# Kernel tuning notes

Measured on AMD Instinct MI355X. Metric: run time of the kernel, lower is better.

Reference implementation:

```python
import jax, jax.numpy as jnp
import numpy as np

H = 512; W = 512; C_IN = 14; HID = 128; N_CELLS = 8192

def _rn(k, shape, sc=0.05):
    return jax.random.normal(k, shape, jnp.float32) * sc

def setup_inputs() -> dict:
    key = jax.random.key(0)
    ks = jax.random.split(key, 32)
    inp = {
        'x': jax.random.normal(ks[0], (1, C_IN, H, W), jnp.float32),
        'cell_i': jax.random.randint(ks[1], (N_CELLS,), 0, H, jnp.int32),
        'cell_j': jax.random.randint(ks[2], (N_CELLS,), 0, W, jnp.int32),
        'action': jax.random.randint(ks[3], (N_CELLS, 4), 0, 2, jnp.int32),
        'w1': _rn(ks[4], (48, C_IN, 3, 3)), 'b1': _rn(ks[5], (48,)),
        'g1': jnp.ones((48,), jnp.float32), 'be1': jnp.zeros((48,), jnp.float32),
        'w2': _rn(ks[6], (96, 48, 3, 3)), 'b2': _rn(ks[7], (96,)),
        'g2': jnp.ones((96,), jnp.float32), 'be2': jnp.zeros((96,), jnp.float32),
        'w3': _rn(ks[8], (HID, 96, 3, 3)), 'b3': _rn(ks[9], (HID,)),
        'g3': jnp.ones((HID,), jnp.float32), 'be3': jnp.zeros((HID,), jnp.float32),
        'fw1': _rn(ks[10], (HID * 9, 256)), 'fb1': _rn(ks[11], (256,)),
        'fw2': _rn(ks[12], (256, 128)), 'fb2': _rn(ks[13], (128,)),
        'bw': _rn(ks[14], (128, 4)), 'bb': _rn(ks[15], (4,)),
        'iw': _rn(ks[16], (128, 4)), 'ib': _rn(ks[17], (4,)),
        'tw': _rn(ks[18], (128, 4)), 'tb': _rn(ks[19], (4,)),
        'vw1': _rn(ks[20], (HID, 64)), 'vb1': _rn(ks[21], (64,)),
        'vw2': _rn(ks[22], (64, 1)), 'vb2': _rn(ks[23], (1,)),
    }
    return inp

def _conv(x, w, b):
    y = jax.lax.conv_general_dilated(x, w, (1, 1), 'SAME',
                                     dimension_numbers=('NCHW', 'OIHW', 'NCHW'))
    return y + b[None, :, None, None]

def _gn(x, gamma, beta, groups, eps=1e-5):
    n, c, h, w = x.shape
    xr = x.reshape(n, groups, -1)
    m = xr.mean(axis=2, keepdims=True)
    v = xr.var(axis=2, keepdims=True)
    xn = ((xr - m) * jax.lax.rsqrt(v + eps)).reshape(n, c, h, w)
    return xn * gamma[None, :, None, None] + beta[None, :, None, None]

def _forward(x, cell_i, cell_j, action, w1, b1, g1, be1, w2, b2, g2, be2,
             w3, b3, g3, be3, fw1, fb1, fw2, fb2, bw, bb, iw, ib, tw, tb,
             vw1, vb1, vw2, vb2):
    # Encoder: conv -> GN -> ReLU x3
    f = jax.nn.relu(_gn(_conv(x, w1, b1), g1, be1, 6))
    f = jax.nn.relu(_gn(_conv(f, w2, b2), g2, be2, 12))
    f = jax.nn.relu(_gn(_conv(f, w3, b3), g3, be3, 16))  # (1, HID, H, W)
    # Value head: global avg pool -> MLP
    pooled = f.mean(axis=(2, 3))  # (1, HID)
    value = jax.nn.relu(pooled @ vw1 + vb1) @ vw2 + vb2  # (1, 1)
    # Per-burning-cell 3x3 patch gather (zero-padded borders)
    fpad = jnp.pad(f, ((0, 0), (0, 0), (1, 1), (1, 1)))[0]  # (HID, H+2, W+2)
    def slice_patch(i, j):
        return jax.lax.dynamic_slice(fpad, (0, i, j), (HID, 3, 3))
    patches = jax.vmap(slice_patch)(cell_i, cell_j)  # (N, HID, 3, 3)
    flat = patches.reshape(patches.shape[0], HID * 9)
    shared = jax.nn.relu(jax.nn.relu(flat @ fw1 + fb1) @ fw2 + fb2)  # (N, 128)
    burn_logits = shared @ bw + bb
    intensity = shared @ iw + ib
    temp = shared @ tw + tb
    p = jnp.clip(jax.nn.sigmoid(burn_logits), 1e-7, 1.0 - 1e-7)
    a = action.astype(jnp.float32)
    log_prob = jnp.sum(a * jnp.log(p) + (1.0 - a) * jnp.log(1.0 - p))
    entropy = -jnp.sum(p * jnp.log(p) + (1.0 - p) * jnp.log(1.0 - p))
    # Scatter sampled actions into grid at N/E/S/W neighbors (in-bounds only)
    di = jnp.array([-1, 0, 1, 0], jnp.int32)
    dj = jnp.array([0, 1, 0, -1], jnp.int32)
    ni = cell_i[:, None] + di
    nj = cell_j[:, None] + dj
    valid = (ni >= 0) & (ni < H) & (nj >= 0) & (nj < W) & (a > 0.5)
    grid = jnp.zeros((H, W), jnp.float32).at[
        jnp.clip(ni, 0, H - 1), jnp.clip(nj, 0, W - 1)].max(valid.astype(jnp.float32))
    return grid, log_prob, entropy, value, intensity, temp

def reference(x, cell_i, cell_j, action, w1, b1, g1, be1, w2, b2, g2, be2,
              w3, b3, g3, be3, fw1, fb1, fw2, fb2, bw, bb, iw, ib, tw, tb,
              vw1, vb1, vw2, vb2):
    return _forward(x, cell_i, cell_j, action, w1, b1, g1, be1, w2, b2, g2, be2,
                    w3, b3, g3, be3, fw1, fb1, fw2, fb2, bw, bb, iw, ib, tw, tb,
                    vw1, vb1, vw2, vb2)
```

## Files before the change

### kernel.cpp

```cpp
#include <hip/hip_runtime.h>
#include <hip/hip_bf16.h>
#include <cstddef>

#define NPIX 262144
#define PW 514
typedef __hip_bfloat16 bf16;
typedef __attribute__((ext_vector_type(8))) short short8;
typedef __attribute__((ext_vector_type(4))) float f32x4;

__device__ inline unsigned short f2bfu(float f){
  __hip_bfloat16 h = __float2bfloat16(f);
  return *(reinterpret_cast<unsigned short*>(&h));
}
__device__ inline float bflo(unsigned u){ return __uint_as_float(u<<16); }
__device__ inline float bfhi(unsigned u){ return __uint_as_float(u & 0xffff0000u); }
__device__ inline unsigned pack2bf(float a, float b){
  unsigned ua = __float_as_uint(a), ub = __float_as_uint(b);
  return ((ua + 0x8000u) >> 16) | ((ub + 0x8000u) & 0xffff0000u);
}
__device__ inline void dma16(const bf16* g, unsigned short* l){
  __builtin_amdgcn_global_load_lds(
      (const __attribute__((address_space(1))) unsigned int*)g,
      (__attribute__((address_space(3))) unsigned int*)l, 16, 0, 0);
}

__device__ inline void computeAB(const float* stats, const float* gamma, const float* beta,
                                 int c, float& A, float& B){
  int g = c >> 3;
  const float invN = 1.f/2097152.f;
  float m = stats[g*2]*invN;
  float v = stats[g*2+1]*invN - m*m;
  float inv = rsqrtf(v + 1e-5f);
  A = inv*gamma[c];
  B = beta[c] - m*A;
}

__global__ void setup_kernel(float* out, float* stats, float* pooled,
                             const float* __restrict__ w1, bf16* __restrict__ wT1,
                             const float* __restrict__ w2, bf16* __restrict__ wT2,
                             const float* __restrict__ w3, bf16* __restrict__ wT3,
                             const float* __restrict__ fw1, bf16* __restrict__ wF1T,
                             const float* __restrict__ fw2, bf16* __restrict__ wF2T){
  int b = blockIdx.x;
  if (b < 1025){
    int i = b*256 + threadIdx.x;
    if (i < 262147) out[i] = 0.f;
    if (i < 68)  stats[i]  = 0.f;
    if (i < 128) pooled[i] = 0.f;
    return;
  }
  b -= 1025;
  if (b < 30){
    int idx = b*256 + threadIdx.x;
    if (idx < 5*48*32){
      int kp = idx & 31; int oc = (idx >> 5) % 48; int kc = idx / (48*32);
      int k = kc*32 + kp;
      int tap = k >> 4, c = k & 15;
      float v = (tap < 9 && c < 14) ? w1[(oc*14 + c)*9 + tap] : 0.f;
      wT1[idx] = __float2bfloat16(v);
    }
    return;
  }
  b -= 30;
  if (b < 216){
    int idx = b*256 + threadIdx.x;
    if (idx < 9*2*96*32){
      int cp = idx & 31; int rest = idx >> 5;
      int oc = rest % 96; rest /= 96;
      int cc = rest % 2; int tap = rest / 2;
      int ic = cc*32 + cp;
      float v = (ic < 48) ? w2[(oc*48 + ic)*9 + tap] : 0.f;
      wT2[idx] = __float2bfloat16(v);
    }
    return;
  }
  b -= 216;
  if (b < 432){
    int idx = b*256 + threadIdx.x;
    if (idx < 9*3*128*32){
      int cp = idx & 31; int rest = idx >> 5;
      int oc = rest & 127; rest >>= 7;
      int cc = rest % 3; int tap = rest / 3;
      int ic = cc*32 + cp;
      float v = (ic < 96) ? w3[(oc*96 + ic)*9 + tap] : 0.f;
      wT3[idx] = __float2bfloat16(v);
    }
    return;
  }
  b -= 432;
  if (b < 1152){
    int idx = b*256 + threadIdx.x;
    if (idx < 36*256*32){
      int kp = idx & 31; int oc = (idx >> 5) & 255; int kc = idx >> 13;
      int k2 = kc*32 + kp;
      int rr = k2 >> 7, ch = k2 & 127;
      wF1T[idx] = __float2bfloat16(fw1[(size_t)(ch*9 + rr)*256 + oc]);
    }
    return;
  }
  b -= 1152;
  {
    int idx = b*256 + threadIdx.x;
    if (idx < 8*128*32){
      int kp = idx & 31; int oc = (idx >> 5) & 127; int kc = idx >> 12;
      wF2T[idx] = __float2bfloat16(fw2[(size_t)(kc*32 + kp)*128 + oc]);
    }
  }
}

__launch_bounds__(256,2)
__global__ void conv1_mfma_kernel(const float* __restrict__ x, const bf16* __restrict__ wT,
                                  const float* __restrict__ bias, bf16* __restrict__ out,
                                  float* __restrict__ stats){
  constexpr int XP = 24;
  __shared__ unsigned short sX[324*XP];
  __shared__ float sStat[96];
  const int tid = threadIdx.x;
  const int lane = tid & 63, wave = tid >> 6;
  const int quad = lane >> 4, l15 = lane & 15;
  const int tileX = (blockIdx.x & 31)*16, tileY = (blockIdx.x >> 5)*16;
  if (tid < 96) sStat[tid] = 0.f;
  for (int p = tid; p < 324; p += 256){ sX[p*XP+14] = 0; sX[p*XP+15] = 0; }
  for (int idx = tid; idx < 14*324; idx += 256){
    int c = idx / 324, p = idx - c*324;
    int r = p / 18, col = p - r*18;
    int gy = tileY + r - 1, gx = tileX + col - 1;
    float v = 0.f;
    if ((unsigned)gy < 512u && (unsigned)gx < 512u) v = x[(size_t)c*NPIX + gy*512 + gx];
    sX[p*XP + c] = f2bfu(v);
  }
  __syncthreads();

  f32x4 acc[3][4];
  #pragma unroll
  for (int t = 0; t < 3; ++t){
    f32x4 bv = *(const f32x4*)(bias + t*16 + quad*4);
    #pragma unroll
    for (int s = 0; s < 4; ++s) acc[t][s] = bv;
  }
  const int pxb = wave*4;
  const int h = quad >> 1, chalf = (quad & 1)*8;
  const int T0[5] = {0,2,4,6,8};
  const int T1[5] = {1,3,5,7,8};
  #pragma unroll
  for (int kc = 0; kc < 5; ++kc){
    short8 a[3];
    #pragma unroll
    for (int t = 0; t < 3; ++t)
      a[t] = *(const short8*)((const unsigned short*)wT + (size_t)(kc*48 + t*16 + l15)*32 + quad*8);
    const int ky = h ? (T1[kc]/3) : (T0[kc]/3);
    const int kx = h ? (T1[kc]%3) : (T0[kc]%3);
    #pragma unroll
    for (int s = 0; s < 4; ++s){
      int py = pxb + s;
      short8 bfr = *(const short8*)(&sX[((py+ky)*18 + l15+kx)*XP + chalf]);
      #pragma unroll
      for (int t = 0; t < 3; ++t)
        acc[t][s] = __builtin_amdgcn_mfma_f32_16x16x32_bf16(a[t], bfr, acc[t][s], 0, 0, 0);
    }
  }
  #pragma unroll
  for (int t = 0; t < 3; ++t){
    #pragma unroll
    for (int r = 0; r < 4; ++r){
      float sv = 0.f, sq = 0.f;
      #pragma unroll
      for (int s = 0; s < 4; ++s){ float v = acc[t][s][r]; sv += v; sq += v*v; }
      #pragma unroll
      for (int m = 1; m < 16; m <<= 1){ sv += __shfl_xor(sv, m); sq += __shfl_xor(sq, m); }
      if (l15 == 0){
        atomicAdd(&sStat[(t*16 + quad*4 + r)*2],   sv);
        atomicAdd(&sStat[(t*16 + quad*4 + r)*2+1], sq);
      }
    }
    #pragma unroll
    for (int s = 0; s < 4; ++s){
      f32x4 v = acc[t][s];
      uint2 pk;
      pk.x = pack2bf(v[0], v[1]);
      pk.y = pack2bf(v[2], v[3]);
      *(uint2*)(out + ((size_t)(tileY+pxb+s+1)*PW + tileX+l15+1)*48 + t*16 + quad*4) = pk;
    }
  }
  __syncthreads();
  if (tid < 12){
    int g = tid >> 1, wsel = tid & 1;
    float v = 0.f;
    #pragma unroll
    for (int j = 0; j < 8; ++j) v += sStat[(g*8+j)*2 + wsel];
    atomicAdd(&stats[g*2 + wsel], v);
  }
}

template<int C>
__global__ void norm_kernel(bf16* buf, const float* __restrict__ stats,
                            const float* __restrict__ gamma, const float* __restrict__ beta){
  __shared__ float sAB[2*C];
  const int tid = threadIdx.x;
  if (tid < C){ float A,B; computeAB(stats, gamma, beta, tid, A, B); sAB[tid]=A; sAB[C+tid]=B; }
  __syncthreads();
  const int y = blockIdx.x >> 2, q = blockIdx.x & 3;
  uint4* row = (uint4*)(buf + (size_t)y*PW*C);
  constexpr int NU4 = PW*C/8/4;
  const bool brow = (y == 0) | (y == 513);
  for (int i = q*NU4 + tid; i < (q+1)*NU4; i += 256){
    int e = i*8;
    int px = e / C;
    if (brow | (px == 0) | (px == 513)){ row[i] = make_uint4(0,0,0,0); continue; }
    int ch = e - px*C;
    uint4 v = row[i];
    unsigned uu[4] = {v.x,v.y,v.z,v.w}, ou[4];
    #pragma unroll
    for (int j = 0; j < 4; ++j){
      float a = fmaxf(bflo(uu[j])*sAB[ch+j*2]   + sAB[C+ch+j*2],   0.f);
      float d = fmaxf(bfhi(uu[j])*sAB[ch+j*2+1] + sAB[C+ch+j*2+1], 0.f);
      ou[j] = pack2bf(a, d);
    }
    row[i] = make_uint4(ou[0],ou[1],ou[2],ou[3]);
  }
}

template<int IC, int NCC, int OCT, int OC, int NW, int TH>
__launch_bounds__(NW*64, 3)
__global__ void conv_dma_kernel(const bf16* __restrict__ in, const bf16* __restrict__ wT,
                                const float* __restrict__ bias,
                                bf16* __restrict__ out, float* __restrict__ outstats){
  constexpr int NT   = NW*64;
  constexpr int ROWS = TH + 2;
  constexpr int SLOTS = ROWS * 72;
  constexpr int K    = (SLOTS + NT - 1) / NT;
  constexpr int REM  = SLOTS - (K-1)*NT;
  __shared__ unsigned short sIn[2][SLOTS*8];
  __shared__ float sStat[2*OC];
  const int tid  = threadIdx.x;
  const int lane = tid & 63, wave = tid >> 6;
  const int quad = lane >> 4, l15 = lane & 15;
  const int tileX = (blockIdx.x & 31) * 16, tileY = (blockIdx.x >> 5) * TH;
  const int ocbase = wave * (OCT*16);

  for (int i = tid; i < 2*OC; i += NT) sStat[i] = 0.f;

  unsigned off[K];
  #pragma unroll
  for (int k = 0; k < K; ++k){
    int slot = tid + k*NT;
    if (k < K-1 || tid < REM){
      int row = slot/72; int rem = slot - row*72;
      int cc = rem/18;   int col = rem - cc*18;
      off[k] = (unsigned)(((tileY+row)*PW + tileX+col)*IC + cc*8);
    }
  }
  auto issueDMA = [&](int cr, int bi){
    #pragma unroll
    for (int k = 0; k < K; ++k){
      if (k == K-1 && tid >= REM) continue;
      dma16(in + off[k] + cr*32, &sIn[bi][(tid + k*NT)*8]);
    }
  };

  f32x4 acc[OCT][TH];
  #pragma unroll
  for (int t = 0; t < OCT; ++t){
    f32x4 bv = *(const f32x4*)(bias + ocbase + t*16 + quad*4);
    #pragma unroll
    for (int s = 0; s < TH; ++s) acc[t][s] = bv;
  }

  issueDMA(0, 0);
  __syncthreads();

  #pragma unroll 1
  for (int cr = 0; cr < NCC; ++cr){
    if (cr + 1 < NCC) issueDMA(cr + 1, (cr + 1) & 1);
    const unsigned short* B0 = &sIn[cr & 1][(quad*18 + l15)*8];
    const unsigned short* W0 = (const unsigned short*)wT + ((size_t)cr*OC + ocbase + l15)*32 + quad*8;

    #pragma unroll
    for (int kx = 0; kx < 3; ++kx){
      short8 a[3][OCT];
      #pragma unroll
      for (int ky = 0; ky < 3; ++ky)
        #pragma unroll
        for (int t = 0; t < OCT; ++t)
          a[ky][t] = *(const short8*)(W0 + (size_t)(ky*3+kx)*(NCC*OC*32) + t*512);
      #pragma unroll
      for (int r = 0; r < ROWS; ++r){
        short8 b = *(const short8*)(B0 + (r*72 + kx)*8);
        #pragma unroll
        for (int ky = 0; ky < 3; ++ky){
          const int s = r - ky;
          if (s >= 0 && s < TH){
            #pragma unroll
            for (int t = 0; t < OCT; ++t)
              acc[t][s] = __builtin_amdgcn_mfma_f32_16x16x32_bf16(a[ky][t], b, acc[t][s], 0, 0, 0);
          }
        }
      }
    }
    __syncthreads();
  }

  #pragma unroll
  for (int t = 0; t < OCT; ++t){
    #pragma unroll
    for (int r = 0; r < 4; ++r){
      float sv = 0.f, sq = 0.f;
      #pragma unroll
      for (int s = 0; s < TH; ++s){ float v = acc[t][s][r]; sv += v; sq += v*v; }
      #pragma unroll
      for (int m = 1; m < 16; m <<= 1){ sv += __shfl_xor(sv, m); sq += __shfl_xor(sq, m); }
      if (l15 == 0){
        atomicAdd(&sStat[(ocbase + t*16 + quad*4 + r)*2],   sv);
        atomicAdd(&sStat[(ocbase + t*16 + quad*4 + r)*2+1], sq);
      }
    }
    #pragma unroll
    for (int s = 0; s < TH; ++s){
      f32x4 v = acc[t][s];
      uint2 pk;
      pk.x = pack2bf(v[0], v[1]);
      pk.y = pack2bf(v[2], v[3]);
      *(uint2*)(out + ((size_t)(tileY+s+1)*PW + (tileX+l15+1))*OC + ocbase + t*16 + quad*4) = pk;
    }
  }
  __syncthreads();
  if (tid < (OC/8)*2){
    int g = tid >> 1, wsel = tid & 1;
    float v = 0.f;
    #pragma unroll
    for (int j = 0; j < 8; ++j) v += sStat[(g*8+j)*2 + wsel];
    atomicAdd(&outstats[g*2 + wsel], v);
  }
}

__launch_bounds__(256)
__global__ void mega_kernel(const bf16* __restrict__ f, const float* __restrict__ instats,
                            const float* __restrict__ gamma, const float* __restrict__ beta,
                            const int* __restrict__ cell_i, const int* __restrict__ cell_j,
                            const int* __restrict__ action,
                            const bf16* __restrict__ wT, const float* __restrict__ fb1,
                            const bf16* __restrict__ wT2, const float* __restrict__ fb2,
                            const float* __restrict__ bw, const float* __restrict__ bb,
                            const float* __restrict__ iw, const float* __restrict__ ib,
                            const float* __restrict__ tw, const float* __restrict__ tb,
                            float* __restrict__ pooled, float* __restrict__ out){
  constexpr int KST = 1160;
  __shared__ unsigned short sG[16*KST];
  __shared__ unsigned short h1L[16*264];
  __shared__ float sAB[256];
  __shared__ int sij[32];
  __shared__ float sRed[2];
  __shared__ float sP[128];
  float* h2L = (float*)sG;
  const int tid = threadIdx.x;
  const int lane = tid & 63, wave = tid >> 6;
  const int quad = lane >> 4, l15 = lane & 15;
  const int cb = blockIdx.x*16;

  if (tid < 2) sRed[tid] = 0.f;
  if (tid < 128){ float A,B; computeAB(instats, gamma, beta, tid, A, B);
    sAB[tid]=A; sAB[128+tid]=B; sP[tid]=0.f; }
  if (tid < 16) sij[tid] = cell_i[cb + tid];
  else if (tid < 32) sij[tid] = cell_j[cb + tid - 16];
  __syncthreads();

  for (int idx = tid; idx < 16*144; idx += 256){
    int c8 = idx & 15; int t2 = idx >> 4;
    int cell = t2 / 9, rr = t2 - cell*9;
    int r = rr/3, cl = rr - r*3;
    int py = sij[cell] + r, px = sij[16+cell] + cl;
    uint4 v = *(const uint4*)(f + ((size_t)py*PW + px)*128 + c8*8);
    bool border = (py==0) | (py==513) | (px==0) | (px==513);
    unsigned uu[4] = {v.x, v.y, v.z, v.w};
    unsigned ou[4];
    #pragma unroll
    for (int j = 0; j < 4; ++j){
      int ch = c8*8 + j*2;
      float a = border ? 0.f : fmaxf(bflo(uu[j])*sAB[ch]   + sAB[128+ch],   0.f);
      float d = border ? 0.f : fmaxf(bfhi(uu[j])*sAB[ch+1] + sAB[128+ch+1], 0.f);
      ou[j] = pack2bf(a, d);
    }
    uint4 wv; wv.x = ou[0]; wv.y = ou[1]; wv.z = ou[2]; wv.w = ou[3];
    *(uint4*)(&sG[cell*KST + rr*128 + c8*8]) = wv;
  }
  __syncthreads();

  {
    f32x4 acc[4];
    const int ocb = wave*64;
    #pragma unroll
    for (int t = 0; t < 4; ++t)
      acc[t] = *(const f32x4*)(fb1 + ocb + t*16 + quad*4);
    #pragma unroll 2
    for (int kc = 0; kc < 36; ++kc){
      short8 b = *(const short8*)(&sG[l15*KST + kc*32 + quad*8]);
      #pragma unroll
      for (int t = 0; t < 4; ++t){
        short8 a = *(const short8*)((const unsigned short*)wT + ((size_t)kc*256 + ocb + t*16 + l15)*32 + quad*8);
        acc[t] = __builtin_amdgcn_mfma_f32_16x16x32_bf16(a, b, acc[t], 0, 0, 0);
      }
    }
    #pragma unroll
    for (int t = 0; t < 4; ++t){
      f32x4 v = acc[t];
      uint2 pk;
      pk.x = pack2bf(fmaxf(v[0],0.f), fmaxf(v[1],0.f));
      pk.y = pack2bf(fmaxf(v[2],0.f), fmaxf(v[3],0.f));
      *(uint2*)(&h1L[l15*264 + ocb + t*16 + quad*4]) = pk;
    }
  }
  __syncthreads();

  {
    const int och = wave*32;
    f32x4 acc2[2];
    #pragma unroll
    for (int t = 0; t < 2; ++t)
      acc2[t] = *(const f32x4*)(fb2 + och + t*16 + quad*4);
    #pragma unroll
    for (int kc = 0; kc < 8; ++kc){
      short8 b = *(const short8*)(&h1L[l15*264 + kc*32 + quad*8]);
      #pragma unroll
      for (int t = 0; t < 2; ++t){
        short8 a = *(const short8*)((const unsigned short*)wT2 + ((size_t)kc*128 + och + t*16 + l15)*32 + quad*8);
        acc2[t] = __builtin_amdgcn_mfma_f32_16x16x32_bf16(a, b, acc2[t], 0, 0, 0);
      }
    }
    #pragma unroll
    for (int t = 0; t < 2; ++t){
      f32x4 v = acc2[t];
      #pragma unroll
      for (int r = 0; r < 4; ++r) v[r] = fmaxf(v[r], 0.f);
      *(f32x4*)(&h2L[l15*132 + och + t*16 + quad*4]) = v;
    }
  }
  __syncthreads();

  if (tid < 192){
    int cell = tid/12, jj = tid - cell*12;
    int which = jj >> 2, o = jj & 3;
    const float* W  = (which==0) ? bw : (which==1 ? iw : tw);
    const float* Bp = (which==0) ? bb : (which==1 ? ib : tb);
    float d = Bp[o];
    const float* h2 = &h2L[cell*132];
    for (int k = 0; k < 128; k++) d += h2[k]*W[k*4+o];
    int cellg = cb + cell;
    if (which == 1){
      out[262147 + cellg*4 + o] = d;
    } else if (which == 2){
      out[262147 + 32768 + cellg*4 + o] = d;
    } else {
      float p = 1.f/(1.f + __expf(-d));
      p = fminf(fmaxf(p, 1e-7f), 1.f - 1e-7f);
      int a = action[cellg*4 + o];
      float lp  = a ? __logf(p) : __logf(1.f-p);
      float ent = -(p*__logf(p) + (1.f-p)*__logf(1.f-p));
      atomicAdd(&sRed[0], lp);
      atomicAdd(&sRed[1], ent);
      if (a){
        const int di[4] = {-1,0,1,0};
        const int dj[4] = {0,1,0,-1};
        int ni = sij[cell] + di[o];
        int nj = sij[16+cell] + dj[o];
        if ((unsigned)ni < 512u && (unsigned)nj < 512u)
          out[ni*512 + nj] = 1.0f;
      }
    }
  }

  {
    const int gl = tid & 15, xl = tid >> 4;
    float A[8], B[8];
    #pragma unroll
    for (int j = 0; j < 8; ++j){ A[j] = sAB[gl*8+j]; B[j] = sAB[128+gl*8+j]; }
    const int y = blockIdx.x;
    float ps[8] = {0,0,0,0,0,0,0,0};
    for (int x2 = xl; x2 < 512; x2 += 16){
      uint4 v = *(const uint4*)(f + ((size_t)(y+1)*PW + x2+1)*128 + gl*8);
      unsigned uu[4] = {v.x, v.y, v.z, v.w};
      #pragma unroll
      for (int j = 0; j < 4; ++j){
        ps[j*2]   += fmaxf(bflo(uu[j])*A[j*2]   + B[j*2],   0.f);
        ps[j*2+1] += fmaxf(bfhi(uu[j])*A[j*2+1] + B[j*2+1], 0.f);
      }
    }
    #pragma unroll
    for (int j = 0; j < 8; ++j) atomicAdd(&sP[gl*8+j], ps[j]);
  }
  __syncthreads();
  if (tid == 0){
    atomicAdd(&out[262144], sRed[0]);
    atomicAdd(&out[262145], sRed[1]);
  }
  if (tid < 128) atomicAdd(&pooled[tid], sP[tid]);
}

__global__ void value_kernel(const float* __restrict__ pooled, const float* __restrict__ vw1,
                             const float* __restrict__ vb1, const float* __restrict__ vw2,
                             const float* __restrict__ vb2, float* __restrict__ out){
  int t = threadIdx.x;
  float h = vb1[t];
  const float invN = 1.f/262144.f;
  for (int c = 0; c < 128; c++) h += (pooled[c]*invN)*vw1[c*64+t];
  h = fmaxf(h, 0.f);
  float v = h*vw2[t];
  #pragma unroll
  for (int off = 32; off; off >>= 1) v += __shfl_xor(v, off);
  if (t == 0) out[262146] = v + vb2[0];
}

extern "C" void kernel_launch(void* const* d_in, const int* in_sizes, int n_in,
                              void* d_out, int out_size, void* d_ws, size_t ws_size,
                              hipStream_t stream) {
  (void)in_sizes; (void)n_in; (void)out_size; (void)ws_size;
  const float* x      = (const float*)d_in[0];
  const int*  cell_i  = (const int*)d_in[1];
  const int*  cell_j  = (const int*)d_in[2];
  const int*  action  = (const int*)d_in[3];
  const float* w1 = (const float*)d_in[4];  const float* b1 = (const float*)d_in[5];
  const float* g1 = (const float*)d_in[6];  const float* be1= (const float*)d_in[7];
  const float* w2 = (const float*)d_in[8];  const float* b2 = (const float*)d_in[9];
  const float* g2 = (const float*)d_in[10]; const float* be2= (const float*)d_in[11];
  const float* w3 = (const float*)d_in[12]; const float* b3 = (const float*)d_in[13];
  const float* g3 = (const float*)d_in[14]; const float* be3= (const float*)d_in[15];
  const float* fw1= (const float*)d_in[16]; const float* fb1= (const float*)d_in[17];
  const float* fw2= (const float*)d_in[18]; const float* fb2= (const float*)d_in[19];
  const float* bw = (const float*)d_in[20]; const float* bb = (const float*)d_in[21];
  const float* iw = (const float*)d_in[22]; const float* ib = (const float*)d_in[23];
  const float* tw = (const float*)d_in[24]; const float* tb = (const float*)d_in[25];
  const float* vw1= (const float*)d_in[26]; const float* vb1= (const float*)d_in[27];
  const float* vw2= (const float*)d_in[28]; const float* vb2= (const float*)d_in[29];

  float* out = (float*)d_out;
  char* ws = (char*)d_ws;
  bf16* buf1 = (bf16*)(ws);
  bf16* buf2 = (bf16*)(ws + 25362816);
  bf16* bufF = (bf16*)(ws + 76088448);
  bf16* wT2  = (bf16*)(ws + 143722624);
  bf16* wT3  = (bf16*)(ws + 143833216);
  bf16* wT1  = (bf16*)(ws + 144054400);
  bf16* wF1T = (bf16*)(ws + 144069760);
  bf16* wF2T = (bf16*)(ws + 144659584);
  float* statsf = (float*)(ws + 144725120);
  float* pooled = statsf + 128;

  setup_kernel<<<2983, 256, 0, stream>>>(out, statsf, pooled, w1, wT1, w2, wT2, w3, wT3,
                                         fw1, wF1T, fw2, wF2T);
  conv1_mfma_kernel<<<1024, 256, 0, stream>>>(x, wT1, b1, buf1, statsf + 0);
  norm_kernel<48><<<514*4, 256, 0, stream>>>(buf1, statsf + 0, g1, be1);
  conv_dma_kernel<48,2,2,96,3,8><<<2048, 192, 0, stream>>>(buf1, wT2, b2, buf2, statsf + 12);
  norm_kernel<96><<<514*4, 256, 0, stream>>>(buf2, statsf + 12, g2, be2);
  conv_dma_kernel<96,3,2,128,4,8><<<2048, 256, 0, stream>>>(buf2, wT3, b3, bufF, statsf + 36);
  mega_kernel<<<512, 256, 0, stream>>>(bufF, statsf + 36, g3, be3, cell_i, cell_j, action,
                                       wF1T, fb1, wF2T, fb2, bw, bb, iw, ib, tw, tb,
                                       pooled, out);
  value_kernel<<<1, 64, 0, stream>>>(pooled, vw1, vb1, vw2, vb2, out);
}
```

Before: 361.2 us.

## Fuse GroupNorm+ReLU into conv input loading, drop separate norm kernels

Removes the two standalone norm_kernel passes and applies the GroupNorm affine and ReLU to the input tile while it is staged into LDS inside the conv kernels. The async global_load_lds DMA is replaced by register loads, a transform, and LDS stores, with the chunk loop manually pipelined and s_setprio raised around the MFMA section. Border zeroing moves into setup_kernel, and padding pixels are forced to zero during staging. This saves two full read-modify-write passes over the large activation buffers, at the cost of higher register pressure, extra ALU work per conv tile, and losing the asynchronous DMA path. Occupancy for conv2 is lowered to 2.

Measured after the change: 439.6 us. 1.22x slower.

```diff
diff --git a/kernel.cpp b/kernel.cpp
--- a/kernel.cpp
+++ b/kernel.cpp
@@ -17,11 +17,6 @@
 __device__ inline unsigned pack2bf(float a, float b){
   unsigned ua = __float_as_uint(a), ub = __float_as_uint(b);
   return ((ua + 0x8000u) >> 16) | ((ub + 0x8000u) & 0xffff0000u);
-}
-__device__ inline void dma16(const bf16* g, unsigned short* l){
-  __builtin_amdgcn_global_load_lds(
-      (const __attribute__((address_space(1))) unsigned int*)g,
-      (__attribute__((address_space(3))) unsigned int*)l, 16, 0, 0);
 }
 
 __device__ inline void computeAB(const float* stats, const float* gamma, const float* beta,
@@ -40,7 +35,8 @@
                              const float* __restrict__ w2, bf16* __restrict__ wT2,
                              const float* __restrict__ w3, bf16* __restrict__ wT3,
                              const float* __restrict__ fw1, bf16* __restrict__ wF1T,
-                             const float* __restrict__ fw2, bf16* __restrict__ wF2T){
+                             const float* __restrict__ fw2, bf16* __restrict__ wF2T,
+                             bf16* __restrict__ bufB1, bf16* __restrict__ bufB2){
   int b = blockIdx.x;
   if (b < 1025){
     int i = b*256 + threadIdx.x;
@@ -99,11 +95,41 @@
     return;
   }
   b -= 1152;
-  {
+  if (b < 128){
     int idx = b*256 + threadIdx.x;
     if (idx < 8*128*32){
       int kp = idx & 31; int oc = (idx >> 5) & 127; int kc = idx >> 12;
       wF2T[idx] = __float2bfloat16(fw2[(size_t)(kc*32 + kp)*128 + oc]);
+    }
+    return;
+  }
+  b -= 128;
+  {
+    int u = b*256 + threadIdx.x;
+    const uint4 z = make_uint4(0u,0u,0u,0u);
+    if (u < 6168){
+      int row = (u < 3084) ? 0 : 513; int r2 = (u < 3084) ? u : u - 3084;
+      ((uint4*)bufB1)[(size_t)row*3084 + r2] = z;
+      return;
+    }
+    u -= 6168;
+    if (u < 6144){
+      int p = u/6, q = u - p*6;
+      int y = 1 + (p>>1), xx = (p&1) ? 513 : 0;
+      ((uint4*)(bufB1 + ((size_t)y*PW + xx)*48))[q] = z;
+      return;
+    }
+    u -= 6144;
+    if (u < 12336){
+      int row = (u < 6168) ? 0 : 513; int r2 = (u < 6168) ? u : u - 6168;
+      ((uint4*)bufB2)[(size_t)row*6168 + r2] = z;
+      return;
+    }
+    u -= 12336;
+    if (u < 12288){
+      int p = u/12, q = u - p*12;
+      int y = 1 + (p>>1), xx = (p&1) ? 513 : 0;
+      ((uint4*)(bufB2 + ((size_t)y*PW + xx)*96))[q] = z;
     }
   }
 }
@@ -192,46 +218,23 @@
   }
 }
 
-template<int C>
-__global__ void norm_kernel(bf16* buf, const float* __restrict__ stats,
-                            const float* __restrict__ gamma, const float* __restrict__ beta){
-  __shared__ float sAB[2*C];
-  const int tid = threadIdx.x;
-  if (tid < C){ float A,B; computeAB(stats, gamma, beta, tid, A, B); sAB[tid]=A; sAB[C+tid]=B; }
-  __syncthreads();
-  const int y = blockIdx.x >> 2, q = blockIdx.x & 3;
-  uint4* row = (uint4*)(buf + (size_t)y*PW*C);
-  constexpr int NU4 = PW*C/8/4;
-  const bool brow = (y == 0) | (y == 513);
-  for (int i = q*NU4 + tid; i < (q+1)*NU4; i += 256){
-    int e = i*8;
-    int px = e / C;
-    if (brow | (px == 0) | (px == 513)){ row[i] = make_uint4(0,0,0,0); continue; }
-    int ch = e - px*C;
-    uint4 v = row[i];
-    unsigned uu[4] = {v.x,v.y,v.z,v.w}, ou[4];
-    #pragma unroll
-    for (int j = 0; j < 4; ++j){
-      float a = fmaxf(bflo(uu[j])*sAB[ch+j*2]   + sAB[C+ch+j*2],   0.f);
-      float d = fmaxf(bfhi(uu[j])*sAB[ch+j*2+1] + sAB[C+ch+j*2+1], 0.f);
-      ou[j] = pack2bf(a, d);
-    }
-    row[i] = make_uint4(ou[0],ou[1],ou[2],ou[3]);
-  }
-}
-
-template<int IC, int NCC, int OCT, int OC, int NW, int TH>
-__launch_bounds__(NW*64, 3)
+template<int IC, int NCC, int OCT, int OC, int NW, int TH, int MINW>
+__launch_bounds__(NW*64, MINW)
 __global__ void conv_dma_kernel(const bf16* __restrict__ in, const bf16* __restrict__ wT,
                                 const float* __restrict__ bias,
+                                const float* __restrict__ instats,
+                                const float* __restrict__ gamma, const float* __restrict__ beta,
                                 bf16* __restrict__ out, float* __restrict__ outstats){
   constexpr int NT   = NW*64;
   constexpr int ROWS = TH + 2;
   constexpr int SLOTS = ROWS * 72;
   constexpr int K    = (SLOTS + NT - 1) / NT;
   constexpr int REM  = SLOTS - (K-1)*NT;
+  constexpr int CPAD = NCC*32;
+  static_assert(NCC >= 2 && NCC <= 3, "NCC in {2,3}");
   __shared__ unsigned short sIn[2][SLOTS*8];
   __shared__ float sStat[2*OC];
+  __shared__ __align__(16) float sAB2[2*CPAD];
   const int tid  = threadIdx.x;
   const int lane = tid & 63, wave = tid >> 6;
   const int quad = lane >> 4, l15 = lane & 15;
@@ -239,22 +242,52 @@
   const int ocbase = wave * (OCT*16);
 
   for (int i = tid; i < 2*OC; i += NT) sStat[i] = 0.f;
-
-  unsigned off[K];
+  for (int c = tid; c < CPAD; c += NT){
+    float A = 0.f, B = 0.f;
+    if (c < IC) computeAB(instats, gamma, beta, c, A, B);
+    sAB2[2*c] = A; sAB2[2*c+1] = B;
+  }
+
+  unsigned off[K]; int cb2[K]; bool bflag[K];
   #pragma unroll
   for (int k = 0; k < K; ++k){
     int slot = tid + k*NT;
     if (k < K-1 || tid < REM){
       int row = slot/72; int rem = slot - row*72;
       int cc = rem/18;   int col = rem - cc*18;
-      off[k] = (unsigned)(((tileY+row)*PW + tileX+col)*IC + cc*8);
-    }
-  }
-  auto issueDMA = [&](int cr, int bi){
+      int py = tileY + row, px = tileX + col;
+      off[k]   = (unsigned)((py*PW + px)*IC + cc*8);
+      cb2[k]   = cc*16;
+      bflag[k] = (py==0) | (py==513) | (px==0) | (px==513);
+    }
+  }
+
+  uint4 rgA[K], rgB[K];
+  auto issueLoad = [&](int cr, uint4* rg){
     #pragma unroll
     for (int k = 0; k < K; ++k){
       if (k == K-1 && tid >= REM) continue;
-      dma16(in + off[k] + cr*32, &sIn[bi][(tid + k*NT)*8]);
+      rg[k] = *(const uint4*)(in + off[k] + cr*32);
+    }
+  };
+  auto doTransform = [&](int cr, const uint4* rg, int bi){
+    #pragma unroll
+    for (int k = 0; k < K; ++k){
+      if (k == K-1 && tid >= REM) continue;
+      uint4 v = rg[k];
+      unsigned uu[4] = {v.x, v.y, v.z, v.w};
+      unsigned ou[4];
+      const float* ab = &sAB2[cb2[k] + cr*64];
+      #pragma unroll
+      for (int j = 0; j < 4; ++j){
+        f32x4 abv = *(const f32x4*)(ab + j*4);
+        float a = fmaxf(bflo(uu[j])*abv[0] + abv[1], 0.f);
+        float d = fmaxf(bfhi(uu[j])*abv[2] + abv[3], 0.f);
+        ou[j] = pack2bf(a, d);
+      }
+      uint4 wv = bflag[k] ? make_uint4(0u,0u,0u,0u)
+                          : make_uint4(ou[0],ou[1],ou[2],ou[3]);
+      *(uint4*)(&sIn[bi][(tid + k*NT)*8]) = wv;
     }
   };
 
@@ -266,15 +299,10 @@
     for (int s = 0; s < TH; ++s) acc[t][s] = bv;
   }
 
-  issueDMA(0, 0);
-  __syncthreads();
-
-  #pragma unroll 1
-  for (int cr = 0; cr < NCC; ++cr){
-    if (cr + 1 < NCC) issueDMA(cr + 1, (cr + 1) & 1);
-    const unsigned short* B0 = &sIn[cr & 1][(quad*18 + l15)*8];
+  auto computeChunk = [&](int cr, int bi){
+    const unsigned short* B0 = &sIn[bi][(quad*18 + l15)*8];
     const unsigned short* W0 = (const unsigned short*)wT + ((size_t)cr*OC + ocbase + l15)*32 + quad*8;
-
+    __builtin_amdgcn_s_setprio(1);
     #pragma unroll
     for (int kx = 0; kx < 3; ++kx){
       short8 a[3][OCT];
@@ -297,8 +325,24 @@
         }
       }
     }
-    __syncthreads();
-  }
+    __builtin_amdgcn_s_setprio(0);
+  };
+
+  issueLoad(0, rgA);
+  if (NCC > 1) issueLoad(1, rgB);
+  __syncthreads();
+  doTransform(0, rgA, 0);
+  if (NCC > 2) issueLoad(2, rgA);
+  __syncthreads();
+  if (NCC > 1) doTransform(1, rgB, 1);
+  computeChunk(0, 0);
+  if (NCC > 1) __syncthreads();
+  if (NCC > 1){
+    if (NCC > 2) doTransform(2, rgA, 0);
+    computeChunk(1, 1);
+    if (NCC > 2) __syncthreads();
+  }
+  if (NCC > 2) computeChunk(2, 0);
 
   #pragma unroll
   for (int t = 0; t < OCT; ++t){
@@ -544,13 +588,13 @@
   float* statsf = (float*)(ws + 144725120);
   float* pooled = statsf + 128;
 
-  setup_kernel<<<2983, 256, 0, stream>>>(out, statsf, pooled, w1, wT1, w2, wT2, w3, wT3,
-                                         fw1, wF1T, fw2, wF2T);
+  setup_kernel<<<3128, 256, 0, stream>>>(out, statsf, pooled, w1, wT1, w2, wT2, w3, wT3,
+                                         fw1, wF1T, fw2, wF2T, buf1, buf2);
   conv1_mfma_kernel<<<1024, 256, 0, stream>>>(x, wT1, b1, buf1, statsf + 0);
-  norm_kernel<48><<<514*4, 256, 0, stream>>>(buf1, statsf + 0, g1, be1);
-  conv_dma_kernel<48,2,2,96,3,8><<<2048, 192, 0, stream>>>(buf1, wT2, b2, buf2, statsf + 12);
-  norm_kernel<96><<<514*4, 256, 0, stream>>>(buf2, statsf + 12, g2, be2);
-  conv_dma_kernel<96,3,2,128,4,8><<<2048, 256, 0, stream>>>(buf2, wT3, b3, bufF, statsf + 36);
+  conv_dma_kernel<48,2,2,96,3,8,2><<<2048, 192, 0, stream>>>(buf1, wT2, b2, statsf + 0, g1, be1,
+                                                             buf2, statsf + 12);
+  conv_dma_kernel<96,3,2,128,4,8,3><<<2048, 256, 0, stream>>>(buf2, wT3, b3, statsf + 12, g2, be2,
+                                                              bufF, statsf + 36);
   mega_kernel<<<512, 256, 0, stream>>>(bufF, statsf + 36, g3, be3, cell_i, cell_j, action,
                                        wF1T, fb1, wF2T, fb2, bw, bb, iw, ib, tw, tb,
                                        pooled, out);
```

## Prefetch all channel chunks upfront with vmcnt waits instead of double buffering

Applied to the files above, without the earlier changes.

The conv kernel now allocates one LDS buffer per channel chunk (NCC of them) and issues every global-to-LDS DMA at the start. It then waits on partial vmcnt counts and uses barriers that skip the drain before computing each chunk, so later loads overlap with earlier compute and the per-iteration full syncthreads is gone. In exchange it uses more LDS, which may lower occupancy, and the hand-set vmcnt values must match the number of outstanding loads per thread (K per chunk). That matching only holds if no other global loads are in flight, yet the weight loads in computeChunk are also global loads and count toward vmcnt.

After: 352.3 us. 2.5% less time.

```diff
diff --git a/kernel.cpp b/kernel.cpp
--- a/kernel.cpp
+++ b/kernel.cpp
@@ -22,6 +22,17 @@
   __builtin_amdgcn_global_load_lds(
       (const __attribute__((address_space(1))) unsigned int*)g,
       (__attribute__((address_space(3))) unsigned int*)l, 16, 0, 0);
+}
+template<int N> __device__ inline void waitvm(){
+  if constexpr (N == 0) asm volatile("s_waitcnt vmcnt(0)" ::: "memory");
+  else if constexpr (N == 3) asm volatile("s_waitcnt vmcnt(3)" ::: "memory");
+  else if constexpr (N == 4) asm volatile("s_waitcnt vmcnt(4)" ::: "memory");
+  else if constexpr (N == 6) asm volatile("s_waitcnt vmcnt(6)" ::: "memory");
+  else static_assert(N == 0, "unsupported vmcnt");
+}
+__device__ inline void barrier_nodrain(){
+  __builtin_amdgcn_s_barrier();
+  asm volatile("" ::: "memory");
 }
 
 __device__ inline void computeAB(const float* stats, const float* gamma, const float* beta,
@@ -230,7 +241,8 @@
   constexpr int SLOTS = ROWS * 72;
   constexpr int K    = (SLOTS + NT - 1) / NT;
   constexpr int REM  = SLOTS - (K-1)*NT;
-  __shared__ unsigned short sIn[2][SLOTS*8];
+  static_assert(NCC >= 2 && NCC <= 3, "NCC in {2,3}");
+  __shared__ unsigned short sIn[NCC][SLOTS*8];
   __shared__ float sStat[2*OC];
   const int tid  = threadIdx.x;
   const int lane = tid & 63, wave = tid >> 6;
@@ -250,11 +262,11 @@
       off[k] = (unsigned)(((tileY+row)*PW + tileX+col)*IC + cc*8);
     }
   }
-  auto issueDMA = [&](int cr, int bi){
+  auto issueDMA = [&](int cr){
     #pragma unroll
     for (int k = 0; k < K; ++k){
       if (k == K-1 && tid >= REM) continue;
-      dma16(in + off[k] + cr*32, &sIn[bi][(tid + k*NT)*8]);
+      dma16(in + off[k] + cr*32, &sIn[cr][(tid + k*NT)*8]);
     }
   };
 
@@ -266,15 +278,9 @@
     for (int s = 0; s < TH; ++s) acc[t][s] = bv;
   }
 
-  issueDMA(0, 0);
-  __syncthreads();
-
-  #pragma unroll 1
-  for (int cr = 0; cr < NCC; ++cr){
-    if (cr + 1 < NCC) issueDMA(cr + 1, (cr + 1) & 1);
-    const unsigned short* B0 = &sIn[cr & 1][(quad*18 + l15)*8];
+  auto computeChunk = [&](int cr){
+    const unsigned short* B0 = &sIn[cr][(quad*18 + l15)*8];
     const unsigned short* W0 = (const unsigned short*)wT + ((size_t)cr*OC + ocbase + l15)*32 + quad*8;
-
     #pragma unroll
     for (int kx = 0; kx < 3; ++kx){
       short8 a[3][OCT];
@@ -297,7 +303,24 @@
         }
       }
     }
-    __syncthreads();
+  };
+
+  issueDMA(0);
+  issueDMA(1);
+  if constexpr (NCC > 2) issueDMA(2);
+
+  waitvm<K*(NCC-1)>();
+  barrier_nodrain();
+  computeChunk(0);
+
+  waitvm<K*(NCC-2)>();
+  barrier_nodrain();
+  computeChunk(1);
+
+  if constexpr (NCC > 2){
+    waitvm<0>();
+    barrier_nodrain();
+    computeChunk(2);
   }
 
   #pragma unroll
```

## Use 16-row tiles with a 2x2 wave split for the second conv

Applied to the files above, without the earlier changes.

Adds a conv kernel variant for conv2 that processes 16x16 pixel tiles per block. Four waves are split into two output-channel groups of 48 channels and two 8-row pixel halves, with double-buffered DMA staging of the input halo. The larger tile lowers the halo overhead (18 rows loaded for 16 rather than 10 for 8) and halves the number of blocks. In exchange it uses more registers and LDS per block (launch bound of 2 blocks per CU), which may reduce occupancy. The old kernel is renamed and still used for conv3.

New measurement: 353.2 us, median of 3. 2.2% less time.

```diff
diff --git a/kernel.cpp b/kernel.cpp
--- a/kernel.cpp
+++ b/kernel.cpp
@@ -220,11 +220,114 @@
   }
 }
 
+template<int IC, int NCC, int OCT, int OC>
+__launch_bounds__(256, 2)
+__global__ void conv_dma16_kernel(const bf16* __restrict__ in, const bf16* __restrict__ wT,
+                                  const float* __restrict__ bias,
+                                  bf16* __restrict__ out, float* __restrict__ outstats){
+  __shared__ unsigned short sIn[2][1296*8];
+  __shared__ float sStat[2*OC];
+  const int tid  = threadIdx.x;
+  const int lane = tid & 63, wave = tid >> 6;
+  const int quad = lane >> 4, l15 = lane & 15;
+  const int ocg = wave >> 1, pxg = wave & 1;
+  const int tileX = (blockIdx.x & 31) * 16, tileY = (blockIdx.x >> 5) * 16;
+  const int ocbase = ocg * (OCT*16);
+
+  for (int i = tid; i < 2*OC; i += 256) sStat[i] = 0.f;
+
+  unsigned off[6];
+  #pragma unroll
+  for (int k = 0; k < 6; ++k){
+    int slot = tid + k*256;
+    if (k < 5 || tid < 16){
+      int row = slot/72; int rem = slot - row*72;
+      int cc = rem/18;   int col = rem - cc*18;
+      off[k] = (unsigned)(((tileY+row)*PW + tileX+col)*IC + cc*8);
+    }
+  }
+  auto issueDMA = [&](int cr, int bi){
+    #pragma unroll
+    for (int k = 0; k < 6; ++k){
+      if (k == 5 && tid >= 16) continue;
+      dma16(in + off[k] + cr*32, &sIn[bi][(tid + k*256)*8]);
+    }
+  };
+
+  f32x4 acc[OCT][8];
+  #pragma unroll
+  for (int t = 0; t < OCT; ++t){
+    f32x4 bv = *(const f32x4*)(bias + ocbase + t*16 + quad*4);
+    #pragma unroll
+    for (int s = 0; s < 8; ++s) acc[t][s] = bv;
+  }
+
+  issueDMA(0, 0);
+  __syncthreads();
+
+  #pragma unroll 1
+  for (int cr = 0; cr < NCC; ++cr){
+    const unsigned short* B0 = &sIn[cr & 1][(((pxg*8)*4 + quad)*18 + l15)*8];
+    const unsigned short* W0 = (const unsigned short*)wT + ((size_t)cr*OC + ocbase + l15)*32 + quad*8;
+
+    #pragma unroll
+    for (int tap = 0; tap < 9; ++tap){
+      if (tap == 7 && cr + 1 < NCC) issueDMA(cr + 1, (cr + 1) & 1);
+      const int ky = tap/3, kx = tap - ky*3;
+      short8 a[OCT];
+      #pragma unroll
+      for (int t = 0; t < OCT; ++t)
+        a[t] = *(const short8*)(W0 + (size_t)tap*(NCC*OC*32) + t*512);
+      #pragma unroll
+      for (int s = 0; s < 8; ++s){
+        short8 b = *(const short8*)(B0 + ((s+ky)*72 + kx)*8);
+        #pragma unroll
+        for (int t = 0; t < OCT; ++t)
+          acc[t][s] = __builtin_amdgcn_mfma_f32_16x16x32_bf16(a[t], b, acc[t][s], 0, 0, 0);
+      }
+    }
+    __syncthreads();
+  }
+
+  #pragma unroll
+  for (int t = 0; t < OCT; ++t){
+    #pragma unroll
+    for (int r = 0; r < 4; ++r){
+      float sv = 0.f, sq = 0.f;
+      #pragma unroll
+      for (int s = 0; s < 8; ++s){ float v = acc[t][s][r]; sv += v; sq += v*v; }
+      #pragma unroll
+      for (int m = 1; m < 16; m <<= 1){ sv += __shfl_xor(sv, m); sq += __shfl_xor(sq, m); }
+      if (l15 == 0){
+        atomicAdd(&sStat[(ocbase + t*16 + quad*4 + r)*2],   sv);
+        atomicAdd(&sStat[(ocbase + t*16 + quad*4 + r)*2+1], sq);
+      }
+    }
+    #pragma unroll
+    for (int s = 0; s < 8; ++s){
+      int py = pxg*8 + s;
+      f32x4 v = acc[t][s];
+      uint2 pk;
+      pk.x = pack2bf(v[0], v[1]);
+      pk.y = pack2bf(v[2], v[3]);
+      *(uint2*)(out + ((size_t)(tileY+py+1)*PW + (tileX+l15+1))*OC + ocbase + t*16 + quad*4) = pk;
+    }
+  }
+  __syncthreads();
+  if (tid < (OC/8)*2){
+    int g = tid >> 1, wsel = tid & 1;
+    float v = 0.f;
+    #pragma unroll
+    for (int j = 0; j < 8; ++j) v += sStat[(g*8+j)*2 + wsel];
+    atomicAdd(&outstats[g*2 + wsel], v);
+  }
+}
+
 template<int IC, int NCC, int OCT, int OC, int NW, int TH>
 __launch_bounds__(NW*64, 3)
-__global__ void conv_dma_kernel(const bf16* __restrict__ in, const bf16* __restrict__ wT,
-                                const float* __restrict__ bias,
-                                bf16* __restrict__ out, float* __restrict__ outstats){
+__global__ void conv_dma8_kernel(const bf16* __restrict__ in, const bf16* __restrict__ wT,
+                                 const float* __restrict__ bias,
+                                 bf16* __restrict__ out, float* __restrict__ outstats){
   constexpr int NT   = NW*64;
   constexpr int ROWS = TH + 2;
   constexpr int SLOTS = ROWS * 72;
@@ -548,9 +651,9 @@
                                          fw1, wF1T, fw2, wF2T);
   conv1_mfma_kernel<<<1024, 256, 0, stream>>>(x, wT1, b1, buf1, statsf + 0);
   norm_kernel<48><<<514*4, 256, 0, stream>>>(buf1, statsf + 0, g1, be1);
-  conv_dma_kernel<48,2,2,96,3,8><<<2048, 192, 0, stream>>>(buf1, wT2, b2, buf2, statsf + 12);
+  conv_dma16_kernel<48,2,3,96><<<1024, 256, 0, stream>>>(buf1, wT2, b2, buf2, statsf + 12);
   norm_kernel<96><<<514*4, 256, 0, stream>>>(buf2, statsf + 12, g2, be2);
-  conv_dma_kernel<96,3,2,128,4,8><<<2048, 256, 0, stream>>>(buf2, wT3, b3, bufF, statsf + 36);
+  conv_dma8_kernel<96,3,2,128,4,8><<<2048, 256, 0, stream>>>(buf2, wT3, b3, bufF, statsf + 36);
   mega_kernel<<<512, 256, 0, stream>>>(bufF, statsf + 36, g3, be3, cell_i, cell_j, action,
                                        wF1T, fb1, wF2T, fb2, bw, bb, iw, ib, tw, tb,
                                        pooled, out);
```
